# Performance work log

Hardware: AMD Instinct MI355X
Metric: run time of the kernel (lower is better)

Reference implementation:

```python
import jax, jax.numpy as jnp
import numpy as np

O, I, KH, KW = 256, 128, 3, 3
STRIDE, PADDING, DILATION, GROUPS = (1, 1), (1, 1), (1, 1), 1


def setup_inputs() -> dict:
    key = jax.random.key(0)
    kx, kw, kb = jax.random.split(key, 3)
    x = jax.random.normal(kx, (16, I, 112, 112), dtype=jnp.float32)
    # Build a realistic float weight, then quantize+pack exactly like the torch module.
    W = jax.random.normal(kw, (O, I, KH, KW), dtype=jnp.float32) * 0.05
    min_val = jnp.min(W)
    max_val = jnp.max(W)
    scale = (max_val - min_val) / 255.0
    q = jnp.clip(jnp.round((W - min_val) / scale), 0, 255).astype(jnp.uint8).reshape(-1)
    q1 = q[0::2].astype(jnp.float16)
    q2 = q[1::2].astype(jnp.float16)
    # torch promotion: fp16 / fp32 -> fp32, fp16 + fp32 -> fp32, so buffer is fp32
    packed_weight = q1.astype(jnp.float32) + q2.astype(jnp.float32) / jnp.float32(255.0)
    bias = jax.random.normal(kb, (O,), dtype=jnp.float32) * 0.1
    return {
        "x": x,
        "packed_weight": packed_weight,
        "scale_w": scale.astype(jnp.float32),
        "zero_point": min_val.astype(jnp.float32),
        "bias": bias,
    }


def _unpack_weights(packed_weight, scale_w, zero_point):
    q1 = jnp.floor(packed_weight)                       # first code of each pair
    q2 = jnp.clip(jnp.round((packed_weight - q1) * 255.0), 0.0, 255.0)
    # interleave q1, q2 back into the flat code stream
    q = jnp.stack([q1, q2], axis=-1).reshape(-1)        # [O*I*KH*KW]
    w = q.reshape(O, I, KH, KW).astype(jnp.float16)     # torch casts to fp16 here
    return w.astype(jnp.float32) * scale_w + zero_point


def reference(x, packed_weight, scale_w, zero_point, bias):
    w = _unpack_weights(packed_weight, scale_w, zero_point)
    out = jax.lax.conv_general_dilated(
        x, w,
        window_strides=STRIDE,
        padding=[(PADDING[0], PADDING[0]), (PADDING[1], PADDING[1])],
        rhs_dilation=DILATION,
        dimension_numbers=("NCHW", "OIHW", "NCHW"),
        feature_group_count=GROUPS,
    )
    return out + bias[None, :, None, None]
```

## Files before the change

### kernel.cpp

```cpp
#include <hip/hip_runtime.h>


#define C_IN  128
#define H_IN  112
#define W_IN  112
#define HW    (H_IN * W_IN)
#define N_B   16
#define O_C   256
#define P_TOT (N_B * HW)

#define HP    114
#define PLANE (HP * HP * 8)
#define XP_OFF   (1u << 20)
#define XP_BYTES (16u * 16u * 114u * 114u * 8u * 2u)
#define WS_NEED  (XP_OFF + XP_BYTES)

#define DQ_N      (O_C * C_IN * 9 / 2)
#define DQ_BLK    ((DQ_N + 255) / 256)
#define ZB_N      (N_B * 16 * 452)
#define ZB_BLK    ((ZB_N + 255) / 256)
#define PAD_BLK   (2 * H_IN * N_B)
#define PREP_BLK  (DQ_BLK + ZB_BLK + PAD_BLK)

typedef __attribute__((ext_vector_type(8))) short bhalf8;
typedef __attribute__((ext_vector_type(4))) float floatx4;

__device__ __forceinline__ unsigned short f2bf(float f) {
  union { float f; unsigned u; } v; v.f = f;
  return (unsigned short)((v.u + 0x7FFFu + ((v.u >> 16) & 1u)) >> 16);
}

#define GLL16(srcp, ldsp)                                                     \
  __builtin_amdgcn_global_load_lds(                                           \
      (const __attribute__((address_space(1))) unsigned int*)(srcp),          \
      (__attribute__((address_space(3))) unsigned int*)(ldsp), 16, 0, 0)


__global__ void prep_all(const float* __restrict__ pw,
                         const float* __restrict__ scale_p,
                         const float* __restrict__ zp_p,
                         const float* __restrict__ x,
                         unsigned short* __restrict__ Wd,
                         unsigned short* __restrict__ xp) {
  __shared__ unsigned short sh[128][60];
  const int bx  = blockIdx.x;
  const int tid = threadIdx.x;

  if (bx < DQ_BLK) {
    int i = bx * 256 + tid;
    if (i >= DQ_N) return;
    float p = pw[i];
    float s = scale_p[0], z = zp_p[0];
    float q1 = floorf(p);
    float q2 = rintf((p - q1) * 255.0f);
    q2 = fminf(fmaxf(q2, 0.0f), 255.0f);
    float wv[2] = { q1 * s + z, q2 * s + z };
#pragma unroll
    for (int k = 0; k < 2; ++k) {
      int f = 2 * i + k;
      int o = f / 1152;
      int rem = f - o * 1152;
      int c = rem / 9;
      int r = rem - c * 9;
      Wd[((r * 16 + (c >> 3)) * 256 + o) * 8 + (c & 7)] = f2bf(wv[k]);
    }
    return;
  }

  if (bx < DQ_BLK + ZB_BLK) {
    int idx = (bx - DQ_BLK) * 256 + tid;
    if (idx >= ZB_N) return;
    int n    = idx / (16 * 452);
    int rem  = idx - n * (16 * 452);
    int oct  = rem / 452;
    int b    = rem - oct * 452;
    int h, w;
    if      (b < 114) { h = 0;           w = b; }
    else if (b < 228) { h = 113;         w = b - 114; }
    else if (b < 340) { h = b - 228 + 1; w = 0; }
    else              { h = b - 340 + 1; w = 113; }
    bhalf8 z = {0, 0, 0, 0, 0, 0, 0, 0};
    *(bhalf8*)(xp + ((size_t)(n * 16 + oct) * HP + h) * HP * 8 + (size_t)w * 8) = z;
    return;
  }

  {
    int idx = bx - (DQ_BLK + ZB_BLK);
    const int s = idx & 1;
    int rest = idx >> 1;
    const int h = rest % H_IN;
    const int n = rest / H_IN;
    const int w0 = s * 56;

#pragma unroll
    for (int k = 0; k < 7; ++k) {
      int id2 = tid + 256 * k;
      int c  = id2 / 14;
      int wq = id2 - c * 14;
      const float* src = x + (size_t)(n * 128 + c) * HW + h * W_IN + w0 + wq * 4;
      float4 v = *(const float4*)src;
      ushort4 b;
      b.x = f2bf(v.x); b.y = f2bf(v.y); b.z = f2bf(v.z); b.w = f2bf(v.w);
      *(ushort4*)&sh[c][wq * 4] = b;
    }
    __syncthreads();
#pragma unroll
    for (int k = 0; k < 4; ++k) {
      int id2 = tid + 256 * k;
      if (id2 < 896) {
        int oct = id2 / 56;
        int wl  = id2 - oct * 56;
        bhalf8 v;
#pragma unroll
        for (int j = 0; j < 8; ++j) v[j] = (short)sh[oct * 8 + j][wl];
        unsigned short* dst = xp +
            ((size_t)(n * 16 + oct) * HP + (h + 1)) * HP * 8 +
            (size_t)(w0 + wl + 1) * 8;
        *(bhalf8*)dst = v;
      }
    }
  }
}


__global__ __launch_bounds__(512, 2) void conv_fast(
    const unsigned short* __restrict__ xp,
    const unsigned short* __restrict__ Wd,
    const float* __restrict__ bias,
    float* __restrict__ out)
{
  __shared__ unsigned short As[3 * 4 * 256 * 8];
  __shared__ unsigned short Bs[3 * 4 * 128 * 8];

  const int tid  = threadIdx.x;
  const int lane = tid & 63;
  const int wave = tid >> 6;
  const int wm   = wave >> 1;
  const int wn   = wave & 1;
  const int lr   = lane >> 4;
  const int lc   = lane & 15;

  const int bswz = (blockIdx.x & 7) * 196 + (blockIdx.x >> 3);
  const int p0  = bswz * 128;
  const int n   = p0 / HW;
  const int hw0 = p0 - n * HW;

  const int pp  = tid & 127;
  const int hwp = hw0 + pp;
  const int h   = hwp / W_IN;
  const int w   = hwp - h * W_IN;
  const unsigned short* bsrc =
      xp + ((size_t)(n * 16 + (tid >> 7)) * HP + (h + 1)) * HP * 8 +
      (size_t)(w + 1) * 8;

  const unsigned short* asrc = Wd + tid * 8;

  unsigned short* adst = As + wave * 512;
  unsigned short* bdst = Bs + wave * 512;

  const unsigned short* arow = As + lr * 2048 + (wm * 64 + lc) * 8;
  const unsigned short* brow = Bs + lr * 1024 + (wn * 64 + lc) * 8;

  floatx4 acc[4][4];
#pragma unroll
  for (int a = 0; a < 4; ++a)
#pragma unroll
    for (int b = 0; b < 4; ++b)
      acc[a][b] = (floatx4){0.f, 0.f, 0.f, 0.f};

  auto stageA = [&](int t, int buf) {
    int r = t >> 2, q4 = t & 3;
    const unsigned short* s = asrc + (r * 16 + q4 * 4) * 2048;
    GLL16(s,        adst + buf * 8192);
    GLL16(s + 4096, adst + buf * 8192 + 4096);
  };
  auto stageB = [&](int t, int buf) {
    int r = t >> 2, q4 = t & 3;
    int dh = r / 3, dw = r - dh * 3;
    ptrdiff_t off = (ptrdiff_t)(q4 * 4) * PLANE +
                    (ptrdiff_t)((dh - 1) * HP + (dw - 1)) * 8;
    GLL16(bsrc + off, bdst + buf * 4096);
  };

  stageA(0, 0); stageB(0, 0);
  stageA(1, 1); stageB(1, 1);
  asm volatile("s_waitcnt vmcnt(3)" ::: "memory");
  __builtin_amdgcn_s_barrier();

  int buf = 0;
  for (int kt = 0; kt < 34; ++kt) {
    int sbuf = buf + 2; if (sbuf >= 3) sbuf -= 3;
    const unsigned short* ar = arow + buf * 8192;
    const unsigned short* br = brow + buf * 4096;
    bhalf8 af[4], bfv[4];

#pragma unroll
    for (int mi = 0; mi < 4; ++mi) af[mi] = *(const bhalf8*)(ar + mi * 128);
#pragma unroll
    for (int ni = 0; ni < 4; ++ni) bfv[ni] = *(const bhalf8*)(br + ni * 128);
    stageA(kt + 2, sbuf);
    stageB(kt + 2, sbuf);
    __builtin_amdgcn_s_barrier();
    asm volatile("s_waitcnt lgkmcnt(0)" ::: "memory");
    __builtin_amdgcn_sched_barrier(0);
    __builtin_amdgcn_s_setprio(1);
#pragma unroll
    for (int mi = 0; mi < 4; ++mi)
#pragma unroll
      for (int ni = 0; ni < 4; ++ni)
        acc[mi][ni] = __builtin_amdgcn_mfma_f32_16x16x32_bf16(
            af[mi], bfv[ni], acc[mi][ni], 0, 0, 0);
    __builtin_amdgcn_s_setprio(0);
    asm volatile("s_waitcnt vmcnt(3)" ::: "memory");
    __builtin_amdgcn_s_barrier();

    buf = (buf + 1 == 3) ? 0 : buf + 1;
  }

  asm volatile("s_waitcnt vmcnt(0)" ::: "memory");
  __builtin_amdgcn_s_barrier();
#pragma unroll
  for (int kk = 0; kk < 2; ++kk) {
    int b2 = (34 + kk) % 3;
    const unsigned short* ar = arow + b2 * 8192;
    const unsigned short* br = brow + b2 * 4096;
    bhalf8 af[4], bfv[4];
#pragma unroll
    for (int mi = 0; mi < 4; ++mi) af[mi]  = *(const bhalf8*)(ar + mi * 128);
#pragma unroll
    for (int ni = 0; ni < 4; ++ni) bfv[ni] = *(const bhalf8*)(br + ni * 128);
#pragma unroll
    for (int mi = 0; mi < 4; ++mi)
#pragma unroll
      for (int ni = 0; ni < 4; ++ni)
        acc[mi][ni] = __builtin_amdgcn_mfma_f32_16x16x32_bf16(
            af[mi], bfv[ni], acc[mi][ni], 0, 0, 0);
  }

#pragma unroll
  for (int mi = 0; mi < 4; ++mi) {
#pragma unroll
    for (int j = 0; j < 4; ++j) {
      const int o  = wm * 64 + mi * 16 + lr * 4 + j;
      const float bo = bias[o];
      float* orow = out + ((size_t)(n * O_C + o)) * HW + hw0 + wn * 64;
#pragma unroll
      for (int ni = 0; ni < 4; ++ni)
        orow[ni * 16 + lc] = acc[mi][ni][j] + bo;
    }
  }
}


__global__ void dequant_kernel(const float* __restrict__ pw,
                               const float* __restrict__ scale_p,
                               const float* __restrict__ zp_p,
                               unsigned short* __restrict__ Wd) {
  int i = blockIdx.x * 256 + threadIdx.x;
  if (i >= (O_C * C_IN * 9) / 2) return;
  float p = pw[i];
  float s = scale_p[0], z = zp_p[0];
  float q1 = floorf(p);
  float q2 = rintf((p - q1) * 255.0f);
  q2 = fminf(fmaxf(q2, 0.0f), 255.0f);
  float wv[2] = { q1 * s + z, q2 * s + z };
#pragma unroll
  for (int k = 0; k < 2; ++k) {
    int f = 2 * i + k;
    int o = f / 1152;
    int rem = f - o * 1152;
    int c = rem / 9;
    int r = rem - c * 9;
    Wd[(r * O_C + o) * C_IN + c] = f2bf(wv[k]);
  }
}

__global__ __launch_bounds__(256, 2) void conv_kernel(
    const float* __restrict__ x,
    const unsigned short* __restrict__ Wd,
    const float* __restrict__ bias,
    float* __restrict__ out)
{
  __shared__ unsigned short As[128][32];
  __shared__ unsigned short Bs[4][128][8];
  const int tid  = threadIdx.x;
  const int lane = tid & 63;
  const int wave = tid >> 6;
  const int wm   = wave >> 1;
  const int wn   = wave & 1;
  const int p0   = blockIdx.x * 128;
  const int o0   = blockIdx.y * 128;
  const int n    = p0 / HW;
  const int hw0  = p0 - n * HW;
  const int pp = tid & 127;
  const int qh = tid >> 7;
  const int hwp = hw0 + pp;
  const int h  = hwp / W_IN;
  const int w  = hwp - h * W_IN;
  const int xnbase = n * C_IN * HW;
  const int lr = lane >> 4;
  const int lc = lane & 15;
  floatx4 acc[4][4];
#pragma unroll
  for (int a = 0; a < 4; ++a)
#pragma unroll
    for (int b = 0; b < 4; ++b)
      acc[a][b] = (floatx4){0.f, 0.f, 0.f, 0.f};
  for (int r = 0; r < 9; ++r) {
    const int dh = r / 3 - 1;
    const int dw = r % 3 - 1;
    const int ih = h + dh;
    const int iw = w + dw;
    const bool valid = ((unsigned)ih < (unsigned)H_IN) & ((unsigned)iw < (unsigned)W_IN);
    const int xb = xnbase + ih * W_IN + iw;
    const unsigned short* Wr = Wd + r * (O_C * C_IN);
    for (int c0 = 0; c0 < C_IN; c0 += 32) {
      __syncthreads();
#pragma unroll
      for (int j = 0; j < 2; ++j) {
        int sdx  = tid + 256 * j;
        int oo = sdx >> 2;
        int c8 = (sdx & 3) << 3;
        bhalf8 v = *(const bhalf8*)(Wr + (o0 + oo) * C_IN + c0 + c8);
        *(bhalf8*)(&As[oo][c8]) = v;
      }
#pragma unroll
      for (int j = 0; j < 2; ++j) {
        int q = qh + 2 * j;
        bhalf8 v;
        if (valid) {
          const float* xpp = x + xb + (c0 + (q << 3)) * HW;
#pragma unroll
          for (int i = 0; i < 8; ++i) v[i] = (short)f2bf(xpp[i * HW]);
        } else {
#pragma unroll
          for (int i = 0; i < 8; ++i) v[i] = 0;
        }
        *(bhalf8*)(&Bs[q][pp][0]) = v;
      }
      __syncthreads();
      bhalf8 af[4], bfv[4];
#pragma unroll
      for (int mi = 0; mi < 4; ++mi)
        af[mi] = *(const bhalf8*)(&As[wm * 64 + mi * 16 + lc][lr << 3]);
#pragma unroll
      for (int ni = 0; ni < 4; ++ni)
        bfv[ni] = *(const bhalf8*)(&Bs[lr][wn * 64 + ni * 16 + lc][0]);
#pragma unroll
      for (int mi = 0; mi < 4; ++mi)
#pragma unroll
        for (int ni = 0; ni < 4; ++ni)
          acc[mi][ni] = __builtin_amdgcn_mfma_f32_16x16x32_bf16(
              af[mi], bfv[ni], acc[mi][ni], 0, 0, 0);
    }
  }
#pragma unroll
  for (int mi = 0; mi < 4; ++mi) {
#pragma unroll
    for (int j = 0; j < 4; ++j) {
      const int o  = o0 + wm * 64 + mi * 16 + lr * 4 + j;
      const float bo = bias[o];
      float* orow = out + (n * O_C + o) * HW + hw0 + wn * 64;
#pragma unroll
      for (int ni = 0; ni < 4; ++ni)
        orow[ni * 16 + lc] = acc[mi][ni][j] + bo;
    }
  }
}


extern "C" void kernel_launch(void* const* d_in, const int* in_sizes, int n_in,
                              void* d_out, int out_size, void* d_ws, size_t ws_size,
                              hipStream_t stream) {
  const float* x    = (const float*)d_in[0];
  const float* pw   = (const float*)d_in[1];
  const float* sw   = (const float*)d_in[2];
  const float* zp   = (const float*)d_in[3];
  const float* bias = (const float*)d_in[4];
  float* out = (float*)d_out;
  unsigned short* Wd = (unsigned short*)d_ws;

  if (ws_size >= WS_NEED) {
    unsigned short* xp = (unsigned short*)((char*)d_ws + XP_OFF);
    prep_all<<<dim3(PREP_BLK), dim3(256), 0, stream>>>(pw, sw, zp, x, Wd, xp);
    conv_fast<<<dim3(P_TOT / 128), dim3(512), 0, stream>>>(xp, Wd, bias, out);
  } else {
    dequant_kernel<<<dim3((O_C * C_IN * 9 / 2 + 255) / 256), dim3(256), 0, stream>>>(
        pw, sw, zp, Wd);
    dim3 grid(P_TOT / 128, O_C / 128);
    conv_kernel<<<grid, dim3(256), 0, stream>>>(x, Wd, bias, out);
  }
}
```

Measured before the change: 158.8 us.

## Split conv grid into full waves plus a finer-grained tail kernel

The main conv kernel now covers only 1536 tiles of 128 pixels, a multiple of the resident block count. A new kernel, conv_q, handles the remaining 4096 pixels of the last image using 128 blocks of 32 pixels each. This aims to shrink the partial last wave that left most CUs idle. It adds a second launch and a less efficient small-tile kernel that reloads the full weight tile per block.

```diff
diff --git a/kernel.cpp b/kernel.cpp
--- a/kernel.cpp
+++ b/kernel.cpp
@@ -14,6 +14,10 @@
 #define XP_OFF   (1u << 20)
 #define XP_BYTES (16u * 16u * 114u * 114u * 8u * 2u)
 #define WS_NEED  (XP_OFF + XP_BYTES)
+
+#define F_BLK   1536
+#define Q_BLK   128
+#define Q_PX0   (F_BLK * 128)
 
 #define DQ_N      (O_C * C_IN * 9 / 2)
 #define DQ_BLK    ((DQ_N + 255) / 256)
@@ -140,7 +144,7 @@
   const int lr   = lane >> 4;
   const int lc   = lane & 15;
 
-  const int bswz = (blockIdx.x & 7) * 196 + (blockIdx.x >> 3);
+  const int bswz = (blockIdx.x & 7) * 192 + (blockIdx.x >> 3);
   const int p0  = bswz * 128;
   const int n   = p0 / HW;
   const int hw0 = p0 - n * HW;
@@ -247,6 +251,123 @@
 #pragma unroll
       for (int ni = 0; ni < 4; ++ni)
         orow[ni * 16 + lc] = acc[mi][ni][j] + bo;
+    }
+  }
+}
+
+
+__global__ __launch_bounds__(512, 2) void conv_q(
+    const unsigned short* __restrict__ xp,
+    const unsigned short* __restrict__ Wd,
+    const float* __restrict__ bias,
+    float* __restrict__ out)
+{
+  __shared__ unsigned short As[3 * 4 * 256 * 8];
+  __shared__ unsigned short Bs[3 * 4 * 32 * 8];
+
+  const int tid  = threadIdx.x;
+  const int lane = tid & 63;
+  const int wave = tid >> 6;
+  const int wm   = wave >> 1;
+  const int wn   = wave & 1;
+  const int lr   = lane >> 4;
+  const int lc   = lane & 15;
+
+  const int qswz = (blockIdx.x & 7) * 16 + (blockIdx.x >> 3);
+  const int p0  = Q_PX0 + qswz * 32;
+  const int n   = 15;
+  const int hw0 = p0 - n * HW;
+
+  const int lt  = tid & 127;
+  const int pp  = lt & 31;
+  const int hwp = hw0 + pp;
+  const int h   = hwp / W_IN;
+  const int w   = hwp - h * W_IN;
+  const unsigned short* bsrc =
+      xp + ((size_t)(n * 16 + (lt >> 5)) * HP + (h + 1)) * HP * 8 +
+      (size_t)(w + 1) * 8;
+
+  const unsigned short* asrc = Wd + tid * 8;
+
+  unsigned short* adst = As + wave * 512;
+  unsigned short* bdst = Bs + (wave & 1) * 512;
+
+  const unsigned short* arow = As + lr * 2048 + (wm * 64 + lc) * 8;
+  const unsigned short* brow = Bs + lr * 256 + (wn * 16 + lc) * 8;
+
+  floatx4 acc[4];
+#pragma unroll
+  for (int a = 0; a < 4; ++a) acc[a] = (floatx4){0.f, 0.f, 0.f, 0.f};
+
+  auto stageA = [&](int t, int buf) {
+    int r = t >> 2, q4 = t & 3;
+    const unsigned short* s = asrc + (r * 16 + q4 * 4) * 2048;
+    GLL16(s,        adst + buf * 8192);
+    GLL16(s + 4096, adst + buf * 8192 + 4096);
+  };
+  auto stageB = [&](int t, int buf) {
+    int r = t >> 2, q4 = t & 3;
+    int dh = r / 3, dw = r - dh * 3;
+    ptrdiff_t off = (ptrdiff_t)(q4 * 4) * PLANE +
+                    (ptrdiff_t)((dh - 1) * HP + (dw - 1)) * 8;
+    GLL16(bsrc + off, bdst + buf * 1024);
+  };
+
+  stageA(0, 0); stageB(0, 0);
+  stageA(1, 1); stageB(1, 1);
+  asm volatile("s_waitcnt vmcnt(3)" ::: "memory");
+  __builtin_amdgcn_s_barrier();
+
+  int buf = 0;
+  for (int kt = 0; kt < 34; ++kt) {
+    int sbuf = buf + 2; if (sbuf >= 3) sbuf -= 3;
+    const unsigned short* ar = arow + buf * 8192;
+    const unsigned short* br = brow + buf * 1024;
+    bhalf8 af[4], bf;
+
+#pragma unroll
+    for (int mi = 0; mi < 4; ++mi) af[mi] = *(const bhalf8*)(ar + mi * 128);
+    bf = *(const bhalf8*)(br);
+    stageA(kt + 2, sbuf);
+    stageB(kt + 2, sbuf);
+    __builtin_amdgcn_s_barrier();
+    asm volatile("s_waitcnt lgkmcnt(0)" ::: "memory");
+    __builtin_amdgcn_sched_barrier(0);
+    __builtin_amdgcn_s_setprio(1);
+#pragma unroll
+    for (int mi = 0; mi < 4; ++mi)
+      acc[mi] = __builtin_amdgcn_mfma_f32_16x16x32_bf16(af[mi], bf, acc[mi], 0, 0, 0);
+    __builtin_amdgcn_s_setprio(0);
+    asm volatile("s_waitcnt vmcnt(3)" ::: "memory");
+    __builtin_amdgcn_s_barrier();
+
+    buf = (buf + 1 == 3) ? 0 : buf + 1;
+  }
+
+  asm volatile("s_waitcnt vmcnt(0)" ::: "memory");
+  __builtin_amdgcn_s_barrier();
+#pragma unroll
+  for (int kk = 0; kk < 2; ++kk) {
+    int b2 = (34 + kk) % 3;
+    const unsigned short* ar = arow + b2 * 8192;
+    const unsigned short* br = brow + b2 * 1024;
+    bhalf8 af[4], bf;
+#pragma unroll
+    for (int mi = 0; mi < 4; ++mi) af[mi] = *(const bhalf8*)(ar + mi * 128);
+    bf = *(const bhalf8*)(br);
+#pragma unroll
+    for (int mi = 0; mi < 4; ++mi)
+      acc[mi] = __builtin_amdgcn_mfma_f32_16x16x32_bf16(af[mi], bf, acc[mi], 0, 0, 0);
+  }
+
+#pragma unroll
+  for (int mi = 0; mi < 4; ++mi) {
+#pragma unroll
+    for (int j = 0; j < 4; ++j) {
+      const int o  = wm * 64 + mi * 16 + lr * 4 + j;
+      const float bo = bias[o];
+      float* orow = out + ((size_t)(n * O_C + o)) * HW + hw0 + wn * 16;
+      orow[lc] = acc[mi][j] + bo;
     }
   }
 }
@@ -383,7 +504,8 @@
   if (ws_size >= WS_NEED) {
     unsigned short* xp = (unsigned short*)((char*)d_ws + XP_OFF);
     prep_all<<<dim3(PREP_BLK), dim3(256), 0, stream>>>(pw, sw, zp, x, Wd, xp);
-    conv_fast<<<dim3(P_TOT / 128), dim3(512), 0, stream>>>(xp, Wd, bias, out);
+    conv_fast<<<dim3(F_BLK), dim3(512), 0, stream>>>(xp, Wd, bias, out);
+    conv_q<<<dim3(Q_BLK), dim3(512), 0, stream>>>(xp, Wd, bias, out);
   } else {
     dequant_kernel<<<dim3((O_C * C_IN * 9 / 2 + 255) / 256), dim3(256), 0, stream>>>(
         pw, sw, zp, Wd);
```

New measurement: 161.9 us. No clear change (+1.9%).
